# Optimization experiments

Measured on AMD Instinct MI355X. Metric: run time of the kernel, lower is better.

## Reference

```python
import jax, jax.numpy as jnp
import numpy as np
from jax import lax

EPS = 1e-8


def conv2d(x, w, b):
    # x: [B,Cin,H,W], w: [Cout,Cin,3,3], stride 1, SAME padding
    y = lax.conv_general_dilated(x, w, (1, 1), 'SAME',
                                 dimension_numbers=('NCHW', 'OIHW', 'NCHW'))
    return y + b[None, :, None, None]


def leaky(x):
    return jnp.where(x >= 0, x, 0.1 * x)


def setup_inputs() -> dict:
    key = jax.random.key(0)
    ks = jax.random.split(key, 10)
    B, C, H, W, N = 4, 1024, 8, 10, 11
    s = lambda fan: 1.0 / np.sqrt(fan)
    return {
        'out_enc': jax.random.normal(ks[0], (B, C, H, W), jnp.float32),
        'h_track': jax.random.normal(ks[1], (B, C, H, W), jnp.float32),
        'outA_prev': jax.random.normal(ks[2], (B, C, H, W), jnp.float32),
        'memory': jax.random.normal(ks[3], (N, B, C, H, W), jnp.float32),
        'w_conv1': jax.random.normal(ks[4], (C, 2 * C, 3, 3), jnp.float32) * s(2 * C * 9),
        'b_conv1': jnp.zeros((C,), jnp.float32),
        'w_conv2': jax.random.normal(ks[5], (C, C, 3, 3), jnp.float32) * s(C * 9),
        'b_conv2': jnp.zeros((C,), jnp.float32),
        'w_lstm': jax.random.normal(ks[6], (4 * C, 2 * C, 3, 3), jnp.float32) * s(2 * C * 9),
        'b_lstm': jnp.zeros((4 * C,), jnp.float32),
        'w_fc': jax.random.normal(ks[7], (7, C), jnp.float32) * s(C),
        'b_fc': jnp.zeros((7,), jnp.float32),
    }


def reference(out_enc, h_track, outA_prev, memory,
              w_conv1, b_conv1, w_conv2, b_conv2,
              w_lstm, b_lstm, w_fc, b_fc):
    # ---- f1: memory attention (alpha over slots, via channel-dim cosine sim) ----
    # cos over channel dim (torch F.cosine_similarity default dim=1)
    num_a = jnp.einsum('bchw,nbchw->nbhw', outA_prev, memory)
    den_a = (jnp.linalg.norm(outA_prev, axis=1)[None]
             * jnp.linalg.norm(memory, axis=2))  # [N,B,H,W]
    cs_a = num_a / jnp.maximum(den_a, EPS)
    alpha = jax.nn.softmax(cs_a, axis=0)  # exp(cs_i)/sum_j exp(cs_j), [N,B,H,W]

    # ---- beta: per-channel cosine sim over spatial dims, normalized over channels ----
    num_b = jnp.einsum('bchw,nbchw->nbc', h_track, memory)
    den_b = (jnp.linalg.norm(h_track.reshape(*h_track.shape[:2], -1), axis=-1)[None]
             * jnp.linalg.norm(memory.reshape(*memory.shape[:3], -1), axis=-1))  # [N,B,C]
    cs_b = num_b / jnp.maximum(den_b, EPS)
    beta = cs_b / (jnp.sum(cs_b, axis=2, keepdims=True) + EPS)  # [N,B,C]

    # M' = sum_i alpha_i * (beta_i (.) m_i)
    M_dash = jnp.einsum('nbhw,nbc,nbchw->bchw', alpha, beta, memory)

    # ---- guidance2 is identity; fusion convs ----
    temp = jnp.concatenate([out_enc, M_dash], axis=1)  # [B,2C,H,W]
    xA = leaky(conv2d(leaky(conv2d(temp, w_conv1, b_conv1)), w_conv2, b_conv2))

    # ---- ConvLSTM, single time step, zero initial state ----
    C = xA.shape[1]
    h0 = jnp.zeros_like(xA)
    gates = conv2d(jnp.concatenate([xA, h0], axis=1), w_lstm, b_lstm)  # [B,4C,H,W]
    i, f, o, g = jnp.split(gates, 4, axis=1)
    c = jax.nn.sigmoid(i) * jnp.tanh(g)  # f * c0 = 0
    h = jax.nn.sigmoid(o) * jnp.tanh(c)  # [B,C,H,W]

    # ---- global average pool + fc (SE3 head) ----
    gap = h.mean(axis=(-2, -1))  # [B,C]
    absPose = gap @ w_fc.T + b_fc  # [B,7]
    return absPose
```

## Files before the change

kernel.cpp:

```cpp
#include <hip/hip_runtime.h>


typedef _Float16 half8 __attribute__((ext_vector_type(8)));
typedef float f32x4 __attribute__((ext_vector_type(4)));

#define EPSF 1e-8f

__device__ __forceinline__ float sigmoidf_(float x){ return 1.0f/(1.0f+expf(-x)); }

__global__ void k_alpha(const float* __restrict__ outA, const float* __restrict__ mem,
                        float* __restrict__ cs_a){
  int nb = blockIdx.x; int n = nb >> 2; int b = nb & 3;
  int p = threadIdx.x; if (p >= 80) return;
  const float* ma = mem + ((size_t)(n*4+b)*1024)*80 + p;
  const float* aa = outA + ((size_t)b*1024)*80 + p;
  float num=0.f, dm=0.f, da=0.f;
  for (int c=0;c<1024;++c){
    float m = ma[(size_t)c*80]; float a = aa[(size_t)c*80];
    num += a*m; dm += m*m; da += a*a;
  }
  float den = fmaxf(sqrtf(da)*sqrtf(dm), EPSF);
  cs_a[n*320 + b*80 + p] = num/den;
}

__global__ void k_softmax(const float* __restrict__ cs_a, float* __restrict__ alpha){
  int t = threadIdx.x; if (t>=320) return;
  float v[11]; float mx = -1e30f;
  #pragma unroll
  for(int n=0;n<11;++n){ v[n]=cs_a[n*320+t]; mx=fmaxf(mx,v[n]); }
  float s=0.f;
  #pragma unroll
  for(int n=0;n<11;++n){ v[n]=expf(v[n]-mx); s+=v[n]; }
  float inv = 1.0f/s;
  #pragma unroll
  for(int n=0;n<11;++n) alpha[n*320+t]=v[n]*inv;
}

__global__ void k_beta(const float* __restrict__ ht, const float* __restrict__ mem,
                       float* __restrict__ cs_b){
  int nb = blockIdx.x; int n = nb>>2, b = nb&3;
  for (int c = threadIdx.x; c < 1024; c += blockDim.x){
    const float4* h4 = (const float4*)(ht + ((size_t)(b*1024+c))*80);
    const float4* m4 = (const float4*)(mem + ((size_t)((n*4+b)*1024+c))*80);
    float num=0.f, dh=0.f, dm=0.f;
    #pragma unroll 4
    for(int q=0;q<20;++q){
      float4 a=h4[q], m=m4[q];
      num += a.x*m.x+a.y*m.y+a.z*m.z+a.w*m.w;
      dh  += a.x*a.x+a.y*a.y+a.z*a.z+a.w*a.w;
      dm  += m.x*m.x+m.y*m.y+m.z*m.z+m.w*m.w;
    }
    float den = fmaxf(sqrtf(dh)*sqrtf(dm), EPSF);
    cs_b[(size_t)(n*4+b)*1024 + c] = num/den;
  }
}

__global__ void k_betanorm(float* __restrict__ cs_b){
  int nb = blockIdx.x;
  float* base = cs_b + (size_t)nb*1024;
  int t = threadIdx.x;
  float v[4]; float s=0.f;
  #pragma unroll
  for(int i=0;i<4;++i){ v[i]=base[t+256*i]; s+=v[i]; }
  for(int off=32; off; off>>=1) s += __shfl_down(s, off, 64);
  __shared__ float red[4];
  if ((t&63)==0) red[t>>6]=s;
  __syncthreads();
  float tot = red[0]+red[1]+red[2]+red[3];
  float inv = 1.0f/(tot + EPSF);
  #pragma unroll
  for(int i=0;i<4;++i) base[t+256*i] = v[i]*inv;
}

__global__ void k_mdash(const float* __restrict__ alpha, const float* __restrict__ beta,
                        const float* __restrict__ mem, float* __restrict__ md){
  int bc = blockIdx.x; int b = bc >> 10; int c = bc & 1023;
  int p = threadIdx.x; if(p>=80) return;
  float acc=0.f;
  #pragma unroll
  for(int n=0;n<11;++n){
    float al = alpha[n*320 + b*80 + p];
    float be = beta[(size_t)(n*4+b)*1024 + c];
    float m  = mem[(((size_t)(n*4+b)*1024)+c)*80 + p];
    acc += al*be*m;
  }
  md[((size_t)(b*1024)+c)*80 + p] = acc;
}

__global__ void k_im2col(const float* __restrict__ src, _Float16* __restrict__ dst,
                         int Kdst, int col0, int Csrc){
  int b = blockIdx.x; int cbase = blockIdx.y*16;
  for (int e = threadIdx.x; e < 16*720; e += blockDim.x){
    int p = e/144; int r = e - p*144; int cl = r/9; int tap = r - cl*9;
    int kh = tap/3, kw = tap - kh*3;
    int ph = p/10, pw = p - ph*10;
    int h = ph + kh - 1, w = pw + kw - 1;
    int c = cbase + cl;
    float v = 0.f;
    if (h>=0 && h<8 && w>=0 && w<10)
      v = src[((size_t)b*Csrc + c)*80 + h*10 + w];
    dst[((size_t)(b*80 + p))*Kdst + col0 + (size_t)c*9 + tap] = (_Float16)v;
  }
}

__launch_bounds__(256)
__global__ void k_gemm2(const _Float16* __restrict__ A, const float* __restrict__ B,
                        float* __restrict__ C, int N, int lda, int ldb, int hsteps){
  __shared__ __align__(16) _Float16 sA[320*64];
  __shared__ __align__(16) _Float16 sB[64*64];
  int nbase = blockIdx.x * 64;
  int kbase = blockIdx.y * hsteps * 64;
  int t = threadIdx.x;
  int lane = t & 63, wv = t >> 6;
  int wm2 = (wv >> 1), wn2 = (wv & 1);
  int frow = lane & 15, fgrp = lane >> 4;
  f32x4 acc[5][2][2] = {};

  for (int hs = 0; hs < hsteps; ++hs){
    int k = kbase + hs*64;
    #pragma unroll
    for (int i = 0; i < 10; ++i){
      int ci = t + 256*i;
      int row = ci >> 3, seg = ci & 7;
      half8 v = *(const half8*)(A + (size_t)row*lda + k + seg*8);
      *(half8*)&sA[row*64 + ((seg ^ (row & 7))*8)] = v;
    }
    #pragma unroll
    for (int i = 0; i < 2; ++i){
      int ci = t + 256*i;
      int row = ci >> 3, seg = ci & 7;
      const float* bp = B + (size_t)(nbase+row)*ldb + k + seg*8;
      float4 b0 = *(const float4*)bp;
      float4 b1 = *(const float4*)(bp+4);
      half8 bv;
      bv[0]=(_Float16)b0.x; bv[1]=(_Float16)b0.y; bv[2]=(_Float16)b0.z; bv[3]=(_Float16)b0.w;
      bv[4]=(_Float16)b1.x; bv[5]=(_Float16)b1.y; bv[6]=(_Float16)b1.z; bv[7]=(_Float16)b1.w;
      *(half8*)&sB[row*64 + ((seg ^ (row & 7))*8)] = bv;
    }
    __syncthreads();

    half8 bf[2][2];
    #pragma unroll
    for (int j = 0; j < 2; ++j)
      #pragma unroll
      for (int ks = 0; ks < 2; ++ks){
        int r = wn2*32 + j*16 + frow;
        int c = fgrp + 4*ks;
        bf[j][ks] = *(const half8*)&sB[r*64 + ((c ^ (r & 7))*8)];
      }

    #pragma unroll
    for (int mt = 0; mt < 5; ++mt){
      half8 af[2][2];
      #pragma unroll
      for (int i = 0; i < 2; ++i)
        #pragma unroll
        for (int ks = 0; ks < 2; ++ks){
          int r = mt*64 + wm2*32 + i*16 + frow;
          int c = fgrp + 4*ks;
          af[i][ks] = *(const half8*)&sA[r*64 + ((c ^ (r & 7))*8)];
        }
      #pragma unroll
      for (int i = 0; i < 2; ++i)
        #pragma unroll
        for (int j = 0; j < 2; ++j){
          acc[mt][i][j] = __builtin_amdgcn_mfma_f32_16x16x32_f16(af[i][0], bf[j][0], acc[mt][i][j], 0,0,0);
          acc[mt][i][j] = __builtin_amdgcn_mfma_f32_16x16x32_f16(af[i][1], bf[j][1], acc[mt][i][j], 0,0,0);
        }
    }
    __syncthreads();
  }

  #pragma unroll
  for (int mt = 0; mt < 5; ++mt)
    #pragma unroll
    for (int i = 0; i < 2; ++i)
      #pragma unroll
      for (int j = 0; j < 2; ++j)
        #pragma unroll
        for (int r = 0; r < 4; ++r){
          int m = mt*64 + wm2*32 + i*16 + fgrp*4 + r;
          int n = nbase + wn2*32 + j*16 + frow;
          atomicAdd(&C[(size_t)m*N + n], acc[mt][i][j][r]);
        }
}

__global__ void k_post(const float* __restrict__ Cacc, const float* __restrict__ bias,
                       float* __restrict__ y){
  int idx = blockIdx.x*blockDim.x + threadIdx.x;
  if (idx >= 327680) return;
  int p = idx % 80; int rest = idx/80; int c = rest & 1023; int b = rest >> 10;
  float v = Cacc[((size_t)(b*80+p))*1024 + c] + bias[c];
  y[idx] = (v >= 0.f) ? v : 0.1f*v;
}

__global__ void k_lstm(const float* __restrict__ G, const float* __restrict__ bias,
                       float* __restrict__ h){
  int idx = blockIdx.x*blockDim.x + threadIdx.x;
  if (idx >= 327680) return;
  int p = idx % 80; int rest = idx/80; int c = rest & 1023; int b = rest >> 10;
  const float* g0 = G + ((size_t)(b*80+p))*4096;
  float gi = g0[c]        + bias[c];
  float go = g0[c+2048]   + bias[c+2048];
  float gg = g0[c+3072]   + bias[c+3072];
  float cc = sigmoidf_(gi)*tanhf(gg);
  h[idx] = sigmoidf_(go)*tanhf(cc);
}

__global__ void k_gap(const float* __restrict__ h, float* __restrict__ gap){
  int idx = blockIdx.x*blockDim.x + threadIdx.x; if (idx>=4096) return;
  const float4* h4 = (const float4*)(h + (size_t)idx*80);
  float s=0.f;
  #pragma unroll 4
  for(int q=0;q<20;++q){ float4 v=h4[q]; s += v.x+v.y+v.z+v.w; }
  gap[idx] = s*(1.0f/80.0f);
}

__global__ void k_fc(const float* __restrict__ gap, const float* __restrict__ wfc,
                     const float* __restrict__ bfc, float* __restrict__ out){
  int t = threadIdx.x; if (t >= 28) return;
  int b = t/7, j = t - b*7;
  float s = bfc[j];
  for(int c=0;c<1024;++c) s += gap[b*1024+c]*wfc[j*1024+c];
  out[t] = s;
}

extern "C" void kernel_launch(void* const* d_in, const int* in_sizes, int n_in,
                              void* d_out, int out_size, void* d_ws, size_t ws_size,
                              hipStream_t stream) {
  const float* out_enc = (const float*)d_in[0];
  const float* h_track = (const float*)d_in[1];
  const float* outA    = (const float*)d_in[2];
  const float* memory  = (const float*)d_in[3];
  const float* w1  = (const float*)d_in[4];
  const float* b1  = (const float*)d_in[5];
  const float* w2  = (const float*)d_in[6];
  const float* b2  = (const float*)d_in[7];
  const float* wl  = (const float*)d_in[8];
  const float* bl  = (const float*)d_in[9];
  const float* wfc = (const float*)d_in[10];
  const float* bfc = (const float*)d_in[11];
  float* out = (float*)d_out;

  char* ws = (char*)d_ws;
  size_t off = 0;
  auto alloc = [&](size_t bytes)->void*{
    void* p = ws + off; off += (bytes + 255) & ~(size_t)255; return p;
  };
  float* cs_a  = (float*)alloc(3520*4);
  float* alpha = (float*)alloc(3520*4);
  float* cs_b  = (float*)alloc(45056*4);
  float* mdash = (float*)alloc(327680*4);
  float* ybuf  = (float*)alloc(327680*4);
  float* xA    = (float*)alloc(327680*4);
  float* hb    = (float*)alloc(327680*4);
  float* gap   = (float*)alloc(4096*4);
  float* Cacc  = (float*)alloc((size_t)1310720*4);
  _Float16* Abuf = (_Float16*)alloc((size_t)5898240*2);

  k_alpha   <<<44, 128, 0, stream>>>(outA, memory, cs_a);
  k_softmax <<<1, 320, 0, stream>>>(cs_a, alpha);
  k_beta    <<<44, 256, 0, stream>>>(h_track, memory, cs_b);
  k_betanorm<<<44, 256, 0, stream>>>(cs_b);
  k_mdash   <<<4096, 128, 0, stream>>>(alpha, cs_b, memory, mdash);

  k_im2col<<<dim3(4,64), 256, 0, stream>>>(out_enc, Abuf, 18432, 0,    1024);
  k_im2col<<<dim3(4,64), 256, 0, stream>>>(mdash,   Abuf, 18432, 9216, 1024);
  hipMemsetAsync(Cacc, 0, (size_t)327680*4, stream);
  k_gemm2<<<dim3(16,16), 256, 0, stream>>>(Abuf, w1, Cacc, 1024, 18432, 18432, 18);
  k_post<<<1280, 256, 0, stream>>>(Cacc, b1, ybuf);

  k_im2col<<<dim3(4,64), 256, 0, stream>>>(ybuf, Abuf, 9216, 0, 1024);
  hipMemsetAsync(Cacc, 0, (size_t)327680*4, stream);
  k_gemm2<<<dim3(16,16), 256, 0, stream>>>(Abuf, w2, Cacc, 1024, 9216, 9216, 9);
  k_post<<<1280, 256, 0, stream>>>(Cacc, b2, xA);

  k_im2col<<<dim3(4,64), 256, 0, stream>>>(xA, Abuf, 9216, 0, 1024);
  hipMemsetAsync(Cacc, 0, (size_t)1310720*4, stream);
  k_gemm2<<<dim3(64,8), 256, 0, stream>>>(Abuf, wl, Cacc, 4096, 9216, 18432, 18);
  k_lstm<<<1280, 256, 0, stream>>>(Cacc, bl, hb);

  k_gap<<<16, 256, 0, stream>>>(hb, gap);
  k_fc <<<1, 64, 0, stream>>>(gap, wfc, bfc, out);
}
```

Baseline: 764.9 us.

## Skip unused forget gate, use split-K partial buffers, prefetch GEMM tiles, fuse attention kernels

The GEMM kernel now uses 512 threads, register-prefetches the next K tile, and writes split-K partials to separate buffers instead of atomically adding into a memset buffer. Reduction kernels sum the partials and apply the bias and activation. The LSTM GEMM skips the forget-gate columns, which never affect the output under a zero initial state. The alpha reduction is split over channels with atomics, beta and its normalization are fused, and the FC head uses a wave-parallel reduction. In exchange the partial buffers take more workspace and the reduction kernels read more memory.

New measurement: 637.2 us. -16.7%, faster.

```diff
diff --git a/kernel.cpp b/kernel.cpp
--- a/kernel.cpp
+++ b/kernel.cpp
@@ -8,26 +8,35 @@
 
 __device__ __forceinline__ float sigmoidf_(float x){ return 1.0f/(1.0f+expf(-x)); }
 
-__global__ void k_alpha(const float* __restrict__ outA, const float* __restrict__ mem,
-                        float* __restrict__ cs_a){
+__global__ void k_alpha_part(const float* __restrict__ outA, const float* __restrict__ mem,
+                             float* __restrict__ numg, float* __restrict__ dmg,
+                             float* __restrict__ dag){
   int nb = blockIdx.x; int n = nb >> 2; int b = nb & 3;
+  int c0 = blockIdx.y * 128;
   int p = threadIdx.x; if (p >= 80) return;
-  const float* ma = mem + ((size_t)(n*4+b)*1024)*80 + p;
-  const float* aa = outA + ((size_t)b*1024)*80 + p;
+  const float* ma = mem + ((size_t)((n*4+b)*1024 + c0))*80 + p;
+  const float* aa = outA + ((size_t)(b*1024 + c0))*80 + p;
   float num=0.f, dm=0.f, da=0.f;
-  for (int c=0;c<1024;++c){
+  #pragma unroll 8
+  for (int c=0;c<128;++c){
     float m = ma[(size_t)c*80]; float a = aa[(size_t)c*80];
     num += a*m; dm += m*m; da += a*a;
   }
-  float den = fmaxf(sqrtf(da)*sqrtf(dm), EPSF);
-  cs_a[n*320 + b*80 + p] = num/den;
-}
-
-__global__ void k_softmax(const float* __restrict__ cs_a, float* __restrict__ alpha){
+  atomicAdd(&numg[n*320 + b*80 + p], num);
+  atomicAdd(&dmg [n*320 + b*80 + p], dm);
+  if (n == 0) atomicAdd(&dag[b*80 + p], da);
+}
+
+__global__ void k_cs_soft(const float* __restrict__ numg, const float* __restrict__ dmg,
+                          const float* __restrict__ dag, float* __restrict__ alpha){
   int t = threadIdx.x; if (t>=320) return;
+  float sda = sqrtf(dag[t]);
   float v[11]; float mx = -1e30f;
   #pragma unroll
-  for(int n=0;n<11;++n){ v[n]=cs_a[n*320+t]; mx=fmaxf(mx,v[n]); }
+  for(int n=0;n<11;++n){
+    float cs = numg[n*320+t] / fmaxf(sda*sqrtf(dmg[n*320+t]), EPSF);
+    v[n]=cs; mx=fmaxf(mx,cs);
+  }
   float s=0.f;
   #pragma unroll
   for(int n=0;n<11;++n){ v[n]=expf(v[n]-mx); s+=v[n]; }
@@ -36,10 +45,14 @@
   for(int n=0;n<11;++n) alpha[n*320+t]=v[n]*inv;
 }
 
-__global__ void k_beta(const float* __restrict__ ht, const float* __restrict__ mem,
-                       float* __restrict__ cs_b){
+__global__ void k_beta_f(const float* __restrict__ ht, const float* __restrict__ mem,
+                         float* __restrict__ beta){
   int nb = blockIdx.x; int n = nb>>2, b = nb&3;
-  for (int c = threadIdx.x; c < 1024; c += blockDim.x){
+  int t = threadIdx.x;
+  float v[4]; float s=0.f;
+  #pragma unroll
+  for (int i=0;i<4;++i){
+    int c = t + 256*i;
     const float4* h4 = (const float4*)(ht + ((size_t)(b*1024+c))*80);
     const float4* m4 = (const float4*)(mem + ((size_t)((n*4+b)*1024+c))*80);
     float num=0.f, dh=0.f, dm=0.f;
@@ -50,26 +63,16 @@
       dh  += a.x*a.x+a.y*a.y+a.z*a.z+a.w*a.w;
       dm  += m.x*m.x+m.y*m.y+m.z*m.z+m.w*m.w;
     }
-    float den = fmaxf(sqrtf(dh)*sqrtf(dm), EPSF);
-    cs_b[(size_t)(n*4+b)*1024 + c] = num/den;
-  }
-}
-
-__global__ void k_betanorm(float* __restrict__ cs_b){
-  int nb = blockIdx.x;
-  float* base = cs_b + (size_t)nb*1024;
-  int t = threadIdx.x;
-  float v[4]; float s=0.f;
-  #pragma unroll
-  for(int i=0;i<4;++i){ v[i]=base[t+256*i]; s+=v[i]; }
-  for(int off=32; off; off>>=1) s += __shfl_down(s, off, 64);
+    v[i] = num / fmaxf(sqrtf(dh)*sqrtf(dm), EPSF);
+    s += v[i];
+  }
+  for (int off=32; off; off>>=1) s += __shfl_down(s, off, 64);
   __shared__ float red[4];
   if ((t&63)==0) red[t>>6]=s;
   __syncthreads();
-  float tot = red[0]+red[1]+red[2]+red[3];
-  float inv = 1.0f/(tot + EPSF);
-  #pragma unroll
-  for(int i=0;i<4;++i) base[t+256*i] = v[i]*inv;
+  float inv = 1.0f/(red[0]+red[1]+red[2]+red[3] + EPSF);
+  #pragma unroll
+  for (int i=0;i<4;++i) beta[(size_t)nb*1024 + t + 256*i] = v[i]*inv;
 }
 
 __global__ void k_mdash(const float* __restrict__ alpha, const float* __restrict__ beta,
@@ -103,108 +106,124 @@
   }
 }
 
-__launch_bounds__(256)
-__global__ void k_gemm2(const _Float16* __restrict__ A, const float* __restrict__ B,
-                        float* __restrict__ C, int N, int lda, int ldb, int hsteps){
+__launch_bounds__(512)
+__global__ void k_gemm3(const _Float16* __restrict__ A, const float* __restrict__ B,
+                        float* __restrict__ Cp, int ncols, int lda, int ldb,
+                        int hsteps, int nskip_at, int nskip){
   __shared__ __align__(16) _Float16 sA[320*64];
   __shared__ __align__(16) _Float16 sB[64*64];
-  int nbase = blockIdx.x * 64;
-  int kbase = blockIdx.y * hsteps * 64;
+  int ntl = blockIdx.x;
+  int nt  = (ntl < nskip_at) ? ntl : ntl + nskip;
+  int col0 = ntl*64;
+  int kbase = blockIdx.y*hsteps*64;
   int t = threadIdx.x;
   int lane = t & 63, wv = t >> 6;
-  int wm2 = (wv >> 1), wn2 = (wv & 1);
+  int wm2 = wv >> 2, wn2 = wv & 3;
   int frow = lane & 15, fgrp = lane >> 4;
-  f32x4 acc[5][2][2] = {};
-
-  for (int hs = 0; hs < hsteps; ++hs){
-    int k = kbase + hs*64;
-    #pragma unroll
-    for (int i = 0; i < 10; ++i){
-      int ci = t + 256*i;
-      int row = ci >> 3, seg = ci & 7;
-      half8 v = *(const half8*)(A + (size_t)row*lda + k + seg*8);
-      *(half8*)&sA[row*64 + ((seg ^ (row & 7))*8)] = v;
-    }
-    #pragma unroll
-    for (int i = 0; i < 2; ++i){
-      int ci = t + 256*i;
-      int row = ci >> 3, seg = ci & 7;
-      const float* bp = B + (size_t)(nbase+row)*ldb + k + seg*8;
-      float4 b0 = *(const float4*)bp;
-      float4 b1 = *(const float4*)(bp+4);
+  f32x4 acc[5][2] = {};
+
+  const _Float16* Ab = A + kbase;
+  const float*    Bb = B + (size_t)(nt*64)*ldb + kbase;
+  int arow[5], aseg[5];
+  #pragma unroll
+  for (int i=0;i<5;++i){ int ci = t + 512*i; arow[i]=ci>>3; aseg[i]=ci&7; }
+  int brow = t>>3, bseg = t&7;
+
+  half8 ra[5]; float4 rb0, rb1;
+  #pragma unroll
+  for (int i=0;i<5;++i) ra[i] = *(const half8*)(Ab + (size_t)arow[i]*lda + aseg[i]*8);
+  { const float* bp = Bb + (size_t)brow*ldb + bseg*8;
+    rb0 = *(const float4*)bp; rb1 = *(const float4*)(bp+4); }
+
+  for (int hs=0; hs<hsteps; ++hs){
+    half8 na[5]; float4 nb0, nb1;
+    if (hs+1 < hsteps){
+      const _Float16* A2 = Ab + (hs+1)*64;
+      const float*    B2 = Bb + (hs+1)*64;
+      #pragma unroll
+      for (int i=0;i<5;++i) na[i] = *(const half8*)(A2 + (size_t)arow[i]*lda + aseg[i]*8);
+      const float* bp = B2 + (size_t)brow*ldb + bseg*8;
+      nb0 = *(const float4*)bp; nb1 = *(const float4*)(bp+4);
+    }
+    #pragma unroll
+    for (int i=0;i<5;++i)
+      *(half8*)&sA[arow[i]*64 + ((aseg[i] ^ (arow[i]&7))*8)] = ra[i];
+    {
       half8 bv;
-      bv[0]=(_Float16)b0.x; bv[1]=(_Float16)b0.y; bv[2]=(_Float16)b0.z; bv[3]=(_Float16)b0.w;
-      bv[4]=(_Float16)b1.x; bv[5]=(_Float16)b1.y; bv[6]=(_Float16)b1.z; bv[7]=(_Float16)b1.w;
-      *(half8*)&sB[row*64 + ((seg ^ (row & 7))*8)] = bv;
+      bv[0]=(_Float16)rb0.x; bv[1]=(_Float16)rb0.y; bv[2]=(_Float16)rb0.z; bv[3]=(_Float16)rb0.w;
+      bv[4]=(_Float16)rb1.x; bv[5]=(_Float16)rb1.y; bv[6]=(_Float16)rb1.z; bv[7]=(_Float16)rb1.w;
+      *(half8*)&sB[brow*64 + ((bseg ^ (brow&7))*8)] = bv;
     }
     __syncthreads();
 
-    half8 bf[2][2];
-    #pragma unroll
-    for (int j = 0; j < 2; ++j)
-      #pragma unroll
-      for (int ks = 0; ks < 2; ++ks){
-        int r = wn2*32 + j*16 + frow;
-        int c = fgrp + 4*ks;
-        bf[j][ks] = *(const half8*)&sB[r*64 + ((c ^ (r & 7))*8)];
-      }
-
-    #pragma unroll
-    for (int mt = 0; mt < 5; ++mt){
+    half8 bf[2];
+    #pragma unroll
+    for (int ks=0; ks<2; ++ks){
+      int r = wn2*16 + frow;
+      int c = fgrp + 4*ks;
+      bf[ks] = *(const half8*)&sB[r*64 + ((c ^ (r&7))*8)];
+    }
+    #pragma unroll
+    for (int mt=0; mt<5; ++mt){
       half8 af[2][2];
       #pragma unroll
-      for (int i = 0; i < 2; ++i)
+      for (int i=0;i<2;++i)
         #pragma unroll
-        for (int ks = 0; ks < 2; ++ks){
+        for (int ks=0;ks<2;++ks){
           int r = mt*64 + wm2*32 + i*16 + frow;
           int c = fgrp + 4*ks;
-          af[i][ks] = *(const half8*)&sA[r*64 + ((c ^ (r & 7))*8)];
+          af[i][ks] = *(const half8*)&sA[r*64 + ((c ^ (r&7))*8)];
         }
       #pragma unroll
-      for (int i = 0; i < 2; ++i)
-        #pragma unroll
-        for (int j = 0; j < 2; ++j){
-          acc[mt][i][j] = __builtin_amdgcn_mfma_f32_16x16x32_f16(af[i][0], bf[j][0], acc[mt][i][j], 0,0,0);
-          acc[mt][i][j] = __builtin_amdgcn_mfma_f32_16x16x32_f16(af[i][1], bf[j][1], acc[mt][i][j], 0,0,0);
-        }
+      for (int i=0;i<2;++i){
+        acc[mt][i] = __builtin_amdgcn_mfma_f32_16x16x32_f16(af[i][0], bf[0], acc[mt][i],0,0,0);
+        acc[mt][i] = __builtin_amdgcn_mfma_f32_16x16x32_f16(af[i][1], bf[1], acc[mt][i],0,0,0);
+      }
     }
     __syncthreads();
-  }
-
-  #pragma unroll
-  for (int mt = 0; mt < 5; ++mt)
-    #pragma unroll
-    for (int i = 0; i < 2; ++i)
+    #pragma unroll
+    for (int i=0;i<5;++i) ra[i]=na[i];
+    rb0=nb0; rb1=nb1;
+  }
+
+  float* Cw = Cp + (size_t)blockIdx.y*320*ncols;
+  #pragma unroll
+  for (int mt=0;mt<5;++mt)
+    #pragma unroll
+    for (int i=0;i<2;++i)
       #pragma unroll
-      for (int j = 0; j < 2; ++j)
-        #pragma unroll
-        for (int r = 0; r < 4; ++r){
-          int m = mt*64 + wm2*32 + i*16 + fgrp*4 + r;
-          int n = nbase + wn2*32 + j*16 + frow;
-          atomicAdd(&C[(size_t)m*N + n], acc[mt][i][j][r]);
-        }
-}
-
-__global__ void k_post(const float* __restrict__ Cacc, const float* __restrict__ bias,
-                       float* __restrict__ y){
-  int idx = blockIdx.x*blockDim.x + threadIdx.x;
-  if (idx >= 327680) return;
-  int p = idx % 80; int rest = idx/80; int c = rest & 1023; int b = rest >> 10;
-  float v = Cacc[((size_t)(b*80+p))*1024 + c] + bias[c];
-  y[idx] = (v >= 0.f) ? v : 0.1f*v;
-}
-
-__global__ void k_lstm(const float* __restrict__ G, const float* __restrict__ bias,
-                       float* __restrict__ h){
-  int idx = blockIdx.x*blockDim.x + threadIdx.x;
-  if (idx >= 327680) return;
-  int p = idx % 80; int rest = idx/80; int c = rest & 1023; int b = rest >> 10;
-  const float* g0 = G + ((size_t)(b*80+p))*4096;
-  float gi = g0[c]        + bias[c];
-  float go = g0[c+2048]   + bias[c+2048];
-  float gg = g0[c+3072]   + bias[c+3072];
+      for (int r=0;r<4;++r){
+        int m = mt*64 + wm2*32 + i*16 + fgrp*4 + r;
+        int n = col0 + wn2*16 + frow;
+        Cw[(size_t)m*ncols + n] = acc[mt][i][r];
+      }
+}
+
+__global__ void k_post_red(const float* __restrict__ Cp, int splits,
+                           const float* __restrict__ bias, float* __restrict__ y){
+  int tid = blockIdx.x*256 + threadIdx.x; if (tid >= 327680) return;
+  int m = tid >> 10, c = tid & 1023;
+  float s = bias[c];
+  for (int sp=0; sp<splits; ++sp) s += Cp[(size_t)sp*327680 + tid];
+  s = (s >= 0.f) ? s : 0.1f*s;
+  int b = m/80, p = m - (m/80)*80;
+  y[((size_t)(b*1024)+c)*80 + p] = s;
+}
+
+__global__ void k_lstm_red(const float* __restrict__ Cp, const float* __restrict__ bias,
+                           float* __restrict__ h){
+  int tid = blockIdx.x*256 + threadIdx.x; if (tid >= 327680) return;
+  int m = tid >> 10, c = tid & 1023;
+  float gi = bias[c], go = bias[2048+c], gg = bias[3072+c];
+  const float* base = Cp + (size_t)m*3072 + c;
+  #pragma unroll
+  for (int sp=0; sp<8; ++sp){
+    const float* bp = base + (size_t)sp*983040;
+    gi += bp[0]; go += bp[1024]; gg += bp[2048];
+  }
   float cc = sigmoidf_(gi)*tanhf(gg);
-  h[idx] = sigmoidf_(go)*tanhf(cc);
+  int b = m/80, p = m - (m/80)*80;
+  h[((size_t)(b*1024)+c)*80 + p] = sigmoidf_(go)*tanhf(cc);
 }
 
 __global__ void k_gap(const float* __restrict__ h, float* __restrict__ gap){
@@ -218,11 +237,20 @@
 
 __global__ void k_fc(const float* __restrict__ gap, const float* __restrict__ wfc,
                      const float* __restrict__ bfc, float* __restrict__ out){
-  int t = threadIdx.x; if (t >= 28) return;
-  int b = t/7, j = t - b*7;
-  float s = bfc[j];
-  for(int c=0;c<1024;++c) s += gap[b*1024+c]*wfc[j*1024+c];
-  out[t] = s;
+  int wv = threadIdx.x >> 6, lane = threadIdx.x & 63;
+  for (int pair = wv; pair < 28; pair += 8){
+    int b = pair/7, j = pair - (pair/7)*7;
+    const float4* g4 = (const float4*)(gap + b*1024);
+    const float4* w4 = (const float4*)(wfc + j*1024);
+    float s = 0.f;
+    #pragma unroll
+    for (int i=0;i<4;++i){
+      float4 g = g4[lane + 64*i], w = w4[lane + 64*i];
+      s += g.x*w.x + g.y*w.y + g.z*w.z + g.w*w.w;
+    }
+    for (int off=32; off; off>>=1) s += __shfl_down(s, off, 64);
+    if (lane==0) out[pair] = s + bfc[j];
+  }
 }
 
 extern "C" void kernel_launch(void* const* d_in, const int* in_sizes, int n_in,
@@ -247,39 +275,37 @@
   auto alloc = [&](size_t bytes)->void*{
     void* p = ws + off; off += (bytes + 255) & ~(size_t)255; return p;
   };
-  float* cs_a  = (float*)alloc(3520*4);
+  float* attp  = (float*)alloc(7360*4);
   float* alpha = (float*)alloc(3520*4);
-  float* cs_b  = (float*)alloc(45056*4);
+  float* beta  = (float*)alloc(45056*4);
   float* mdash = (float*)alloc(327680*4);
   float* ybuf  = (float*)alloc(327680*4);
   float* xA    = (float*)alloc(327680*4);
   float* hb    = (float*)alloc(327680*4);
   float* gap   = (float*)alloc(4096*4);
-  float* Cacc  = (float*)alloc((size_t)1310720*4);
+  float* Cpart = (float*)alloc((size_t)8*983040*4);
   _Float16* Abuf = (_Float16*)alloc((size_t)5898240*2);
-
-  k_alpha   <<<44, 128, 0, stream>>>(outA, memory, cs_a);
-  k_softmax <<<1, 320, 0, stream>>>(cs_a, alpha);
-  k_beta    <<<44, 256, 0, stream>>>(h_track, memory, cs_b);
-  k_betanorm<<<44, 256, 0, stream>>>(cs_b);
-  k_mdash   <<<4096, 128, 0, stream>>>(alpha, cs_b, memory, mdash);
+  float* numg = attp, *dmg = attp+3520, *dag = attp+7040;
+
+  hipMemsetAsync(attp, 0, 7360*4, stream);
+  k_alpha_part<<<dim3(44,8), 128, 0, stream>>>(outA, memory, numg, dmg, dag);
+  k_cs_soft   <<<1, 320, 0, stream>>>(numg, dmg, dag, alpha);
+  k_beta_f    <<<44, 256, 0, stream>>>(h_track, memory, beta);
+  k_mdash     <<<4096, 128, 0, stream>>>(alpha, beta, memory, mdash);
 
   k_im2col<<<dim3(4,64), 256, 0, stream>>>(out_enc, Abuf, 18432, 0,    1024);
   k_im2col<<<dim3(4,64), 256, 0, stream>>>(mdash,   Abuf, 18432, 9216, 1024);
-  hipMemsetAsync(Cacc, 0, (size_t)327680*4, stream);
-  k_gemm2<<<dim3(16,16), 256, 0, stream>>>(Abuf, w1, Cacc, 1024, 18432, 18432, 18);
-  k_post<<<1280, 256, 0, stream>>>(Cacc, b1, ybuf);
+  k_gemm3<<<dim3(16,16), 512, 0, stream>>>(Abuf, w1, Cpart, 1024, 18432, 18432, 18, 16, 0);
+  k_post_red<<<1280, 256, 0, stream>>>(Cpart, 16, b1, ybuf);
 
   k_im2col<<<dim3(4,64), 256, 0, stream>>>(ybuf, Abuf, 9216, 0, 1024);
-  hipMemsetAsync(Cacc, 0, (size_t)327680*4, stream);
-  k_gemm2<<<dim3(16,16), 256, 0, stream>>>(Abuf, w2, Cacc, 1024, 9216, 9216, 9);
-  k_post<<<1280, 256, 0, stream>>>(Cacc, b2, xA);
+  k_gemm3<<<dim3(16,16), 512, 0, stream>>>(Abuf, w2, Cpart, 1024, 9216, 9216, 9, 16, 0);
+  k_post_red<<<1280, 256, 0, stream>>>(Cpart, 16, b2, xA);
 
   k_im2col<<<dim3(4,64), 256, 0, stream>>>(xA, Abuf, 9216, 0, 1024);
-  hipMemsetAsync(Cacc, 0, (size_t)1310720*4, stream);
-  k_gemm2<<<dim3(64,8), 256, 0, stream>>>(Abuf, wl, Cacc, 4096, 9216, 18432, 18);
-  k_lstm<<<1280, 256, 0, stream>>>(Cacc, bl, hb);
+  k_gemm3<<<dim3(48,8), 512, 0, stream>>>(Abuf, wl, Cpart, 3072, 9216, 18432, 18, 16, 16);
+  k_lstm_red<<<1280, 256, 0, stream>>>(Cpart, bl, hb);
 
   k_gap<<<16, 256, 0, stream>>>(hb, gap);
-  k_fc <<<1, 64, 0, stream>>>(gap, wfc, bfc, out);
-}
+  k_fc <<<1, 512, 0, stream>>>(gap, wfc, bfc, out);
+}
```
